# Kernel tuning notes

Hardware: AMD Instinct MI355X
Metric: run time of the kernel (lower is better)

The kernel has to match this reference:

```python
import jax, jax.numpy as jnp
import numpy as np

B, L, D = 8, 8192, 768
NE = 128
MAX_LEN = 16


def setup_inputs() -> dict:
    key = jax.random.key(0)
    k1, k2, k3, k4, k5 = jax.random.split(key, 5)
    x = jax.random.normal(k1, (B, L, D), dtype=jnp.float32)
    starts = jnp.sort(jax.random.randint(k2, (B, NE), 0, L - MAX_LEN - 1), axis=-1).astype(jnp.int32)
    lengths = jax.random.randint(k3, (B, NE), 1, MAX_LEN + 1).astype(jnp.int32)
    # all i<j entity pairs, same combinatorial structure per document
    iu, ju = np.triu_indices(NE, k=1)
    hts = jnp.broadcast_to(jnp.stack([jnp.asarray(iu), jnp.asarray(ju)], axis=-1).astype(jnp.int32),
                           (B, iu.shape[0], 2))
    threshold = jnp.float32(0.9)
    W1 = jax.random.normal(k4, (1, 128), dtype=jnp.float32) * (1.0)
    b1 = jnp.zeros((128,), dtype=jnp.float32)
    W2 = jax.random.normal(k5, (128, 2), dtype=jnp.float32) * 0.1
    b2 = jnp.zeros((2,), dtype=jnp.float32)
    return {"x": x, "starts": starts, "lengths": lengths, "hts": hts,
            "threshold": threshold, "W1": W1, "b1": b1, "W2": W2, "b2": b2}


def reference(x, starts, lengths, hts, threshold, W1, b1, W2, b2):
    Bd, Ld, Dd = x.shape
    pos = jnp.arange(Ld, dtype=jnp.int32)
    ends = starts + lengths
    # span mask [B, NE, L]; variable-length mean pool via masked matmul
    mask = ((pos[None, None, :] >= starts[:, :, None]) &
            (pos[None, None, :] < ends[:, :, None])).astype(x.dtype)
    cnt = mask.sum(-1, keepdims=True)  # lengths >= 1 by construction
    emb = jnp.einsum('bel,bld->bed', mask, x) / cnt  # [B, NE, D]
    # pairwise cosine similarity (torch eps = 1e-8)
    norms = jnp.linalg.norm(emb, axis=-1)  # [B, NE]
    sim = jnp.einsum('bid,bjd->bij', emb, emb) / jnp.maximum(
        norms[:, :, None] * norms[:, None, :], 1e-8)
    # torch .std() over all elements, unbiased (ddof=1), per document
    std = jnp.std(sim, axis=(1, 2), ddof=1)
    sim_std = (sim - threshold) / (std[:, None, None] + 1e-5)
    # gather i<j pairs in row-major order (matches the nested python loop)
    bidx = jnp.arange(Bd, dtype=jnp.int32)[:, None]
    pairs = sim_std[bidx, hts[:, :, 0], hts[:, :, 1]].reshape(-1, 1)  # [B*P, 1]
    # classifier: Linear(1,128) -> Dropout(eval: identity) -> ReLU -> Linear(128,2)
    h = jax.nn.relu(pairs @ W1 + b1)
    logits = h @ W2 + b2
    return logits
```

## Files before the change

kernel.cpp:

```cpp
#include <hip/hip_runtime.h>
#include <math.h>

#define Bn 8
#define Ln 8192
#define Dn 768
#define NEn 128
#define NPAIR 8128

#define OFF_NORMS  (Bn*NEn*Dn)
#define OFF_SIM    (OFF_NORMS + Bn*NEn)
#define OFF_SUMS_B ((size_t)(OFF_SIM + Bn*NEn*NEn) * 4)

__global__ __launch_bounds__(192) void pool_kernel(
    const float* __restrict__ x, const int* __restrict__ starts,
    const int* __restrict__ lengths, float* __restrict__ emb,
    float* __restrict__ norms, double* __restrict__ sums) {
  int be = blockIdx.x;
  int b  = be >> 7;
  int t  = threadIdx.x;
  if (be == 0 && t < Bn * 2) sums[t] = 0.0;

  int s   = starts[be];
  int len = lengths[be];
  const float4* base = (const float4*)(x + ((size_t)b * Ln + s) * Dn);
  float4 acc = make_float4(0.f, 0.f, 0.f, 0.f);
  for (int r = 0; r < len; ++r) {
    float4 v = base[(size_t)r * 192 + t];
    acc.x += v.x; acc.y += v.y; acc.z += v.z; acc.w += v.w;
  }
  float inv = 1.0f / (float)len;
  acc.x *= inv; acc.y *= inv; acc.z *= inv; acc.w *= inv;
  ((float4*)(emb + (size_t)be * Dn))[t] = acc;

  float ss = acc.x*acc.x + acc.y*acc.y + acc.z*acc.z + acc.w*acc.w;
  for (int off = 32; off; off >>= 1) ss += __shfl_down(ss, off);
  __shared__ float red[3];
  if ((t & 63) == 0) red[t >> 6] = ss;
  __syncthreads();
  if (t == 0) norms[be] = sqrtf(red[0] + red[1] + red[2]);
}

__global__ __launch_bounds__(256) void sim_kernel(
    const float* __restrict__ emb, const float* __restrict__ norms,
    float* __restrict__ sim, double* __restrict__ sums) {
  int bi = blockIdx.x;
  int b  = bi >> 7;
  int t  = threadIdx.x;
  int lane = t & 63;
  int wave = t >> 6;

  __shared__ float4 ei4[192];
  __shared__ float wsum[4], wsq[4];
  const float4* e_i = (const float4*)(emb + (size_t)bi * Dn);
  if (t < 192) ei4[t] = e_i[t];
  __syncthreads();

  float norm_i = norms[bi];
  float lsum = 0.f, lsq = 0.f;
  for (int j = wave; j < NEn; j += 4) {
    const float4* e_j = (const float4*)(emb + ((size_t)(b * NEn + j)) * Dn);
    float dot = 0.f;
#pragma unroll
    for (int c = 0; c < 3; ++c) {
      float4 a = ei4[lane + 64 * c];
      float4 v = e_j[lane + 64 * c];
      dot += a.x*v.x + a.y*v.y + a.z*v.z + a.w*v.w;
    }
    for (int off = 32; off; off >>= 1) dot += __shfl_down(dot, off);
    if (lane == 0) {
      float nj  = norms[b * NEn + j];
      float den = fmaxf(norm_i * nj, 1e-8f);
      float v   = dot / den;
      sim[(size_t)bi * NEn + j] = v;
      lsum += v; lsq += v * v;
    }
  }
  if (lane == 0) { wsum[wave] = lsum; wsq[wave] = lsq; }
  __syncthreads();
  if (t == 0) {
    double s = (double)wsum[0] + wsum[1] + wsum[2] + wsum[3];
    double q = (double)wsq[0]  + wsq[1]  + wsq[2]  + wsq[3];
    atomicAdd(&sums[b * 2 + 0], s);
    atomicAdd(&sums[b * 2 + 1], q);
  }
}

__global__ __launch_bounds__(256) void head_kernel(
    const float* __restrict__ sim, const double* __restrict__ sums,
    const int* __restrict__ hts, const float* __restrict__ thr,
    const float* __restrict__ W1, const float* __restrict__ b1,
    const float* __restrict__ W2, const float* __restrict__ b2,
    float* __restrict__ out) {
  __shared__ float sW1[128], sb1[128], sW2[256];
  int t = threadIdx.x;
  if (t < 128) { sW1[t] = W1[t]; sb1[t] = b1[t]; }
  sW2[t] = W2[t];
  __syncthreads();

  int p = blockIdx.x * 256 + t;
  int b = p / NPAIR;
  int i = hts[(size_t)p * 2];
  int j = hts[(size_t)p * 2 + 1];

  double ssum = sums[b * 2 + 0];
  double ssq  = sums[b * 2 + 1];
  const double N = (double)(NEn * NEn);
  double var  = (ssq - ssum * ssum / N) / (N - 1.0);
  float stdv  = (float)sqrt(var);

  float v = sim[((size_t)b * NEn + i) * NEn + j];
  float s = (v - thr[0]) / (stdv + 1e-5f);

  float acc0 = b2[0], acc1 = b2[1];
#pragma unroll 8
  for (int k = 0; k < 128; ++k) {
    float h = fmaxf(s * sW1[k] + sb1[k], 0.0f);
    acc0 += h * sW2[2 * k];
    acc1 += h * sW2[2 * k + 1];
  }
  ((float2*)out)[p] = make_float2(acc0, acc1);
}

extern "C" void kernel_launch(void* const* d_in, const int* in_sizes, int n_in,
                              void* d_out, int out_size, void* d_ws, size_t ws_size,
                              hipStream_t stream) {
  const float* x       = (const float*)d_in[0];
  const int*   starts  = (const int*)d_in[1];
  const int*   lengths = (const int*)d_in[2];
  const int*   hts     = (const int*)d_in[3];
  const float* thr     = (const float*)d_in[4];
  const float* W1      = (const float*)d_in[5];
  const float* b1      = (const float*)d_in[6];
  const float* W2      = (const float*)d_in[7];
  const float* b2      = (const float*)d_in[8];
  float* out = (float*)d_out;

  float*  emb   = (float*)d_ws;
  float*  norms = emb + OFF_NORMS;
  float*  sim   = emb + OFF_SIM;
  double* sums  = (double*)((char*)d_ws + OFF_SUMS_B);

  pool_kernel<<<Bn * NEn, 192, 0, stream>>>(x, starts, lengths, emb, norms, sums);
  sim_kernel<<<Bn * NEn, 256, 0, stream>>>(emb, norms, sim, sums);
  head_kernel<<<(Bn * NPAIR) / 256, 256, 0, stream>>>(
      sim, sums, hts, thr, W1, b1, W2, b2, out);
}
```

Baseline: 298.0 us.

## Register-tile cosine similarity into 4x2 blocks per lane group

Restructures the similarity kernel so each block computes four query rows against all 128 entities. Each 4-lane group accumulates a 4x2 tile of dot products, with k strided across the lanes. This raises reuse of loaded embedding data and replaces per-entry full-wave reductions with two-step shuffles. It reduces the grid to 256 blocks, which lowers parallelism and latency hiding.

New measurement: 269.8 us. 9.5% less time.

```diff
diff --git a/kernel.cpp b/kernel.cpp
--- a/kernel.cpp
+++ b/kernel.cpp
@@ -43,37 +43,71 @@
 __global__ __launch_bounds__(256) void sim_kernel(
     const float* __restrict__ emb, const float* __restrict__ norms,
     float* __restrict__ sim, double* __restrict__ sums) {
-  int bi = blockIdx.x;
-  int b  = bi >> 7;
-  int t  = threadIdx.x;
+  int blk = blockIdx.x;
+  int b   = blk >> 5;
+  int i0  = (blk & 31) * 4;
+  int t    = threadIdx.x;
   int lane = t & 63;
   int wave = t >> 6;
+  int g    = lane >> 2;
+  int l    = lane & 3;
 
-  __shared__ float4 ei4[192];
+  __shared__ float4 ei4[4 * 193];
   __shared__ float wsum[4], wsq[4];
-  const float4* e_i = (const float4*)(emb + (size_t)bi * Dn);
-  if (t < 192) ei4[t] = e_i[t];
+
+  const float4* embf4 = (const float4*)emb;
+  for (int idx = t; idx < 4 * 192; idx += 256) {
+    int r = idx / 192, c = idx - r * 192;
+    ei4[r * 193 + c] = embf4[(size_t)(b * NEn + i0 + r) * 192 + c];
+  }
   __syncthreads();
 
-  float norm_i = norms[bi];
+  int j0 = wave * 32 + g * 2;
+  const float4* ej0 = embf4 + (size_t)(b * NEn + j0) * 192;
+  const float4* ej1 = ej0 + 192;
+
+  float acc00=0.f, acc01=0.f, acc10=0.f, acc11=0.f;
+  float acc20=0.f, acc21=0.f, acc30=0.f, acc31=0.f;
+#pragma unroll 4
+  for (int k = 0; k < 48; ++k) {
+    float4 e0 = ej0[4 * k + l];
+    float4 e1 = ej1[4 * k + l];
+    float4 a0 = ei4[0 * 193 + 4 * k + l];
+    float4 a1 = ei4[1 * 193 + 4 * k + l];
+    float4 a2 = ei4[2 * 193 + 4 * k + l];
+    float4 a3 = ei4[3 * 193 + 4 * k + l];
+    acc00 += a0.x*e0.x + a0.y*e0.y + a0.z*e0.z + a0.w*e0.w;
+    acc01 += a0.x*e1.x + a0.y*e1.y + a0.z*e1.z + a0.w*e1.w;
+    acc10 += a1.x*e0.x + a1.y*e0.y + a1.z*e0.z + a1.w*e0.w;
+    acc11 += a1.x*e1.x + a1.y*e1.y + a1.z*e1.z + a1.w*e1.w;
+    acc20 += a2.x*e0.x + a2.y*e0.y + a2.z*e0.z + a2.w*e0.w;
+    acc21 += a2.x*e1.x + a2.y*e1.y + a2.z*e1.z + a2.w*e1.w;
+    acc30 += a3.x*e0.x + a3.y*e0.y + a3.z*e0.z + a3.w*e0.w;
+    acc31 += a3.x*e1.x + a3.y*e1.y + a3.z*e1.z + a3.w*e1.w;
+  }
+#define RED(v) v += __shfl_down(v, 1); v += __shfl_down(v, 2);
+  RED(acc00) RED(acc01) RED(acc10) RED(acc11)
+  RED(acc20) RED(acc21) RED(acc30) RED(acc31)
+#undef RED
+
   float lsum = 0.f, lsq = 0.f;
-  for (int j = wave; j < NEn; j += 4) {
-    const float4* e_j = (const float4*)(emb + ((size_t)(b * NEn + j)) * Dn);
-    float dot = 0.f;
+  if (l == 0) {
+    float nj0 = norms[b * NEn + j0];
+    float nj1 = norms[b * NEn + j0 + 1];
+    float dots[4][2] = {{acc00,acc01},{acc10,acc11},{acc20,acc21},{acc30,acc31}};
 #pragma unroll
-    for (int c = 0; c < 3; ++c) {
-      float4 a = ei4[lane + 64 * c];
-      float4 v = e_j[lane + 64 * c];
-      dot += a.x*v.x + a.y*v.y + a.z*v.z + a.w*v.w;
+    for (int i = 0; i < 4; ++i) {
+      float ni = norms[b * NEn + i0 + i];
+      float v0 = dots[i][0] / fmaxf(ni * nj0, 1e-8f);
+      float v1 = dots[i][1] / fmaxf(ni * nj1, 1e-8f);
+      float* row = sim + ((size_t)(b * NEn + i0 + i)) * NEn + j0;
+      row[0] = v0; row[1] = v1;
+      lsum += v0 + v1; lsq += v0*v0 + v1*v1;
     }
-    for (int off = 32; off; off >>= 1) dot += __shfl_down(dot, off);
-    if (lane == 0) {
-      float nj  = norms[b * NEn + j];
-      float den = fmaxf(norm_i * nj, 1e-8f);
-      float v   = dot / den;
-      sim[(size_t)bi * NEn + j] = v;
-      lsum += v; lsq += v * v;
-    }
+  }
+  for (int off = 32; off; off >>= 1) {
+    lsum += __shfl_down(lsum, off);
+    lsq  += __shfl_down(lsq,  off);
   }
   if (lane == 0) { wsum[wave] = lsum; wsq[wave] = lsq; }
   __syncthreads();
@@ -141,7 +175,7 @@
   double* sums  = (double*)((char*)d_ws + OFF_SUMS_B);
 
   pool_kernel<<<Bn * NEn, 192, 0, stream>>>(x, starts, lengths, emb, norms, sums);
-  sim_kernel<<<Bn * NEn, 256, 0, stream>>>(emb, norms, sim, sums);
+  sim_kernel<<<Bn * 32, 256, 0, stream>>>(emb, norms, sim, sums);
   head_kernel<<<(Bn * NPAIR) / 256, 256, 0, stream>>>(
       sim, sums, hts, thr, W1, b1, W2, b2, out);
 }
```
